# Performance work log

Measured on AMD Instinct MI355X. Metric: run time of the kernel, lower is better.

The kernel has to match this reference:

```python
import jax, jax.numpy as jnp
import numpy as np

SMOOTH = 1e-5
ALPHA = 0.25
GAMMA = 2.0
INIT_BETA = 0.5
BETA_DECAY = 0.99


def setup_inputs() -> dict:
    key = jax.random.key(0)
    ks = jax.random.split(key, 7)
    B, NC, C, H, W, D = 8, 1000, 19, 512, 512, 768
    return {
        "logits": jax.random.normal(ks[0], (B, NC), dtype=jnp.float32),
        "label": jax.random.randint(ks[1], (B,), 0, NC),
        "vision_feat": jax.random.normal(ks[2], (B, D), dtype=jnp.float32),
        "text_feat": jax.random.normal(ks[3], (B, D), dtype=jnp.float32),
        "modal_mask": jax.random.uniform(ks[4], (B, 2), dtype=jnp.float32),
        "seg_mask": jax.random.normal(ks[5], (B, C, H, W), dtype=jnp.float32),
        "seg_gt": jax.random.randint(ks[6], (B, H, W), 0, C),
        "epoch": 5,
    }


def _ce_mean(logits, label):
    logp = jax.nn.log_softmax(logits, axis=-1)
    return -jnp.take_along_axis(logp, label[:, None], axis=-1).mean()


def _dice_loss(pred, target):
    # pred: [B,C,H,W] (raw, as in the torch module), target: [B,H,W] int
    C = pred.shape[1]
    onehot = (target[:, None, :, :] == jnp.arange(C)[None, :, None, None]).astype(pred.dtype)
    inter = jnp.sum(pred * onehot, axis=(2, 3))          # [B,C]
    union = jnp.sum(pred, axis=(2, 3)) + jnp.sum(onehot, axis=(2, 3))
    dice = (2.0 * inter + SMOOTH) / (union + SMOOTH)
    return jnp.mean(1.0 - dice)


def _focal_loss(pred, target):
    # pred: [B,C,H,W] logits over class axis 1
    logp = jax.nn.log_softmax(pred, axis=1)
    logp_t = jnp.take_along_axis(logp, target[:, None, :, :], axis=1)[:, 0]  # [B,H,W]
    p_t = jnp.exp(logp_t)
    ce = -logp_t
    return jnp.mean(ALPHA * (1.0 - p_t) ** GAMMA * ce)


def _modal_balance(vision_feat, text_feat, modal_mask, epoch):
    beta_t = INIT_BETA * BETA_DECAY ** epoch
    vn = vision_feat / jnp.linalg.norm(vision_feat, axis=1, keepdims=True)
    tn = text_feat / jnp.linalg.norm(text_feat, axis=1, keepdims=True)
    v_cons = jnp.mean((vn - vn.mean(axis=0, keepdims=True)) ** 2)
    t_cons = jnp.mean((tn - tn.mean(axis=0, keepdims=True)) ** 2)
    cross = 1.0 - jnp.mean(jnp.sum(vn * tn, axis=1))  # cosine sim of unit vectors
    return ((1.0 - beta_t) * v_cons * modal_mask[:, 0].mean()
            + beta_t * t_cons * modal_mask[:, 1].mean() + cross)


def reference(logits, label, vision_feat, text_feat, modal_mask, seg_mask, seg_gt, epoch):
    ce = _ce_mean(logits, label)
    mb = _modal_balance(vision_feat, text_feat, modal_mask, epoch)
    seg = _dice_loss(seg_mask, seg_gt) + _focal_loss(seg_mask, seg_gt)
    total = ce + 0.3 * mb + 0.5 * seg
    return total
```

## Files before the change

kernel.cpp:

```cpp
#include <hip/hip_runtime.h>
#include <math.h>

#define SMOOTH_F 1e-5f
#define ALPHA_F 0.25f

constexpr int Bn = 8;
constexpr int NCn = 1000;
constexpr int Cn = 19;
constexpr int HWn = 512 * 512;
constexpr int Dn = 768;
constexpr int BC = Bn * Cn;

constexpr int TPB = 256;
constexpr int G4 = HWn / 4;
constexpr int BLKS_PER_B = G4 / TPB;
constexpr int SEG_BLOCKS = Bn * BLKS_PER_B;

constexpr int PLANE = SEG_BLOCKS;
constexpr int NPLANES = 3 * Cn + 1;
constexpr int WS_CE = NPLANES * PLANE;
constexpr int WS_MB = WS_CE + 1;

__device__ __forceinline__ float wave_sum(float v) {
#pragma unroll
  for (int off = 32; off > 0; off >>= 1) v += __shfl_down(v, off, 64);
  return v;
}
__device__ __forceinline__ float wave_max(float v) {
#pragma unroll
  for (int off = 32; off > 0; off >>= 1) v = fmaxf(v, __shfl_down(v, off, 64));
  return v;
}

__global__ __launch_bounds__(TPB, 4) void k_seg(
    const float* __restrict__ pred, const int* __restrict__ gt,
    const float* __restrict__ logits, const int* __restrict__ label,
    const float* __restrict__ vf, const float* __restrict__ tf,
    const float* __restrict__ mmask, const int* __restrict__ epoch,
    float* __restrict__ ws) {
  __shared__ float s_inter[Cn];
  __shared__ float s_count[Cn];
  __shared__ float s_pred[Cn];
  __shared__ float s_red[4];
  __shared__ float sA[4];
  __shared__ float sBv[4];
  __shared__ float nv[Bn];
  __shared__ float nt[Bn];

  const int tid = threadIdx.x;
  const int wid = tid >> 6, lane = tid & 63;
  const int blk = blockIdx.x;

  if (blk < 2) {
    if (blk == 0) {
      float acc = 0.0f;
      for (int b = 0; b < Bn; ++b) {
        const float* row = logits + b * NCn;
        float lm = -INFINITY;
        for (int j = tid; j < NCn; j += TPB) lm = fmaxf(lm, row[j]);
        lm = wave_max(lm);
        if (lane == 0) sA[wid] = lm;
        __syncthreads();
        float bm = fmaxf(fmaxf(sA[0], sA[1]), fmaxf(sA[2], sA[3]));
        __syncthreads();
        float ls = 0.0f;
        for (int j = tid; j < NCn; j += TPB) ls += expf(row[j] - bm);
        ls = wave_sum(ls);
        if (lane == 0) sA[wid] = ls;
        __syncthreads();
        if (tid == 0) {
          float lse = bm + logf(sA[0] + sA[1] + sA[2] + sA[3]);
          acc += row[label[b]] - lse;
        }
        __syncthreads();
      }
      if (tid == 0) ws[WS_CE] = -(acc / (float)Bn);
    } else {
      for (int b = 0; b < Bn; ++b) {
        float sv = 0.0f, st = 0.0f;
        for (int j = tid; j < Dn; j += TPB) {
          float a = vf[b * Dn + j];
          float c = tf[b * Dn + j];
          sv += a * a;
          st += c * c;
        }
        sv = wave_sum(sv);
        st = wave_sum(st);
        if (lane == 0) { sA[wid] = sv; sBv[wid] = st; }
        __syncthreads();
        if (tid == 0) {
          nv[b] = sqrtf(sA[0] + sA[1] + sA[2] + sA[3]);
          nt[b] = sqrtf(sBv[0] + sBv[1] + sBv[2] + sBv[3]);
        }
        __syncthreads();
      }
      float colv = 0.0f, colt = 0.0f, cross = 0.0f;
      for (int j = tid; j < Dn; j += TPB) {
        float sv = 0.0f, ssv = 0.0f, stt = 0.0f, sst = 0.0f, cr = 0.0f;
        for (int b = 0; b < Bn; ++b) {
          float vn = vf[b * Dn + j] / nv[b];
          float tn = tf[b * Dn + j] / nt[b];
          sv += vn; ssv += vn * vn;
          stt += tn; sst += tn * tn;
          cr += vn * tn;
        }
        colv += ssv - sv * sv * 0.125f;
        colt += sst - stt * stt * 0.125f;
        cross += cr;
      }
      colv = wave_sum(colv);
      colt = wave_sum(colt);
      cross = wave_sum(cross);
      if (lane == 0) { sA[wid] = colv; sBv[wid] = colt; s_red[wid] = cross; }
      __syncthreads();
      if (tid == 0) {
        float cv = sA[0] + sA[1] + sA[2] + sA[3];
        float ct = sBv[0] + sBv[1] + sBv[2] + sBv[3];
        float cr = s_red[0] + s_red[1] + s_red[2] + s_red[3];
        float v_cons = cv / (float)(Bn * Dn);
        float t_cons = ct / (float)(Bn * Dn);
        float crossv = 1.0f - cr * 0.125f;
        float beta = 0.5f * powf(0.99f, (float)epoch[0]);
        float mm0 = 0.0f, mm1 = 0.0f;
        for (int b = 0; b < Bn; ++b) { mm0 += mmask[b * 2]; mm1 += mmask[b * 2 + 1]; }
        mm0 *= 0.125f; mm1 *= 0.125f;
        ws[WS_MB] = (1.0f - beta) * v_cons * mm0 + beta * t_cons * mm1 + crossv;
      }
    }
    return;
  }

  const int sblk = blk - 2;
  const int b = sblk >> 8;
  const int grp = ((sblk & 255) << 8) + tid;

  const float* base = pred + (size_t)b * Cn * HWn;
  const int* gbase = gt + (size_t)b * HWn;
  const unsigned int goff = ((unsigned int)grp) << 4;

  if (tid < Cn) { s_inter[tid] = 0.0f; s_count[tid] = 0.0f; s_pred[tid] = 0.0f; }
  __syncthreads();

  int4 t4;
  float4 x[Cn];
  asm volatile("global_load_dwordx4 %0, %1, %2"
               : "=v"(t4) : "v"(goff), "s"(gbase));
#pragma unroll
  for (int c = 0; c < Cn; ++c) {
    const unsigned int off = goff + (unsigned int)c * (unsigned int)(HWn * 4);
    asm volatile("global_load_dwordx4 %0, %1, %2"
                 : "=v"(x[c]) : "v"(off), "s"(base));
  }
  asm volatile("s_waitcnt vmcnt(0)");
  __builtin_amdgcn_sched_barrier(0);

  float4 se = make_float4(0.0f, 0.0f, 0.0f, 0.0f);
  float4 xt = make_float4(0.0f, 0.0f, 0.0f, 0.0f);
  float psum[Cn];
#pragma unroll
  for (int c = 0; c < Cn; ++c) {
    const float4 v = x[c];
    psum[c] = v.x + v.y + v.z + v.w;
    se.x += __expf(v.x);
    se.y += __expf(v.y);
    se.z += __expf(v.z);
    se.w += __expf(v.w);
    if (t4.x == c) xt.x = v.x;
    if (t4.y == c) xt.y = v.y;
    if (t4.z == c) xt.z = v.z;
    if (t4.w == c) xt.w = v.w;
  }

  float focal = 0.0f;
#pragma unroll
  for (int j = 0; j < 4; ++j) {
    const float sej = (j == 0) ? se.x : (j == 1) ? se.y : (j == 2) ? se.z : se.w;
    const float xtj = (j == 0) ? xt.x : (j == 1) ? xt.y : (j == 2) ? xt.z : xt.w;
    const int t     = (j == 0) ? t4.x : (j == 1) ? t4.y : (j == 2) ? t4.z : t4.w;
    const float lpt = xtj - __logf(sej);
    const float p = __expf(lpt);
    const float om = 1.0f - p;
    focal += om * om * (-lpt);
    atomicAdd(&s_inter[t], xtj);
    atomicAdd(&s_count[t], 1.0f);
  }

#pragma unroll
  for (int c = 0; c < Cn; ++c) {
    float pc = wave_sum(psum[c]);
    if (lane == 0) atomicAdd(&s_pred[c], pc);
  }
  const float fw = wave_sum(focal * ALPHA_F);
  if (lane == 0) s_red[wid] = fw;
  __syncthreads();

  if (tid < Cn) {
    ws[(size_t)tid * PLANE + sblk] = s_inter[tid];
    ws[(size_t)(Cn + tid) * PLANE + sblk] = s_pred[tid];
    ws[(size_t)(2 * Cn + tid) * PLANE + sblk] = s_count[tid];
  }
  if (tid == 0)
    ws[(size_t)(3 * Cn) * PLANE + sblk] = s_red[0] + s_red[1] + s_red[2] + s_red[3];
}

__global__ __launch_bounds__(1024) void k_final(
    const float* __restrict__ ws, float* __restrict__ out) {
  __shared__ float s_part[912];
  __shared__ float s_d[3];
  __shared__ float s_f;
  const int tid = threadIdx.x;
  const int wid = tid >> 6, lane = tid & 63;

  if (tid < 2 * 3 * BC) {
    const int job = tid >> 1;
    const int half = tid & 1;
    const int quant = job / BC;
    const int pair = job - quant * BC;
    const int b = pair / Cn;
    const int c = pair - b * Cn;
    const float4* p = (const float4*)(ws + (size_t)(quant * Cn + c) * PLANE +
                                      b * 256 + half * 128);
    float s = 0.0f;
#pragma unroll 8
    for (int k = 0; k < 32; ++k) {
      const float4 v = p[k];
      s += v.x + v.y + v.z + v.w;
    }
    s_part[tid] = s;
  }
  if (wid == 15) {
    const float4* p = (const float4*)(ws + (size_t)(3 * Cn) * PLANE) + lane * 8;
    float f = 0.0f;
#pragma unroll
    for (int k = 0; k < 8; ++k) {
      const float4 v = p[k];
      f += v.x + v.y + v.z + v.w;
    }
    f = wave_sum(f);
    if (lane == 0) s_f = f;
  }
  __syncthreads();

  float v = 0.0f;
  if (tid < BC) {
    const float inter = s_part[(0 * BC + tid) * 2] + s_part[(0 * BC + tid) * 2 + 1];
    const float ps    = s_part[(1 * BC + tid) * 2] + s_part[(1 * BC + tid) * 2 + 1];
    const float cnt   = s_part[(2 * BC + tid) * 2] + s_part[(2 * BC + tid) * 2 + 1];
    const float dice = (2.0f * inter + SMOOTH_F) / (ps + cnt + SMOOTH_F);
    v = 1.0f - dice;
  }
  v = wave_sum(v);
  if (lane == 0 && wid < 3) s_d[wid] = v;
  __syncthreads();

  if (tid == 0) {
    const float dice_mean = (s_d[0] + s_d[1] + s_d[2]) / (float)BC;
    const float focal_mean = s_f / (float)(Bn * HWn);
    const float seg = dice_mean + focal_mean;
    out[0] = ws[WS_CE] + 0.3f * ws[WS_MB] + 0.5f * seg;
  }
}

extern "C" void kernel_launch(void* const* d_in, const int* in_sizes, int n_in,
                              void* d_out, int out_size, void* d_ws, size_t ws_size,
                              hipStream_t stream) {
  const float* logits = (const float*)d_in[0];
  const int* label    = (const int*)d_in[1];
  const float* vf     = (const float*)d_in[2];
  const float* tf     = (const float*)d_in[3];
  const float* mmask  = (const float*)d_in[4];
  const float* seg    = (const float*)d_in[5];
  const int* gt       = (const int*)d_in[6];
  const int* epoch    = (const int*)d_in[7];
  float* out = (float*)d_out;
  float* ws = (float*)d_ws;

  hipLaunchKernelGGL(k_seg, dim3(SEG_BLOCKS + 2), dim3(TPB), 0, stream,
                     seg, gt, logits, label, vf, tf, mmask, epoch, ws);
  hipLaunchKernelGGL(k_final, dim3(1), dim3(1024), 0, stream, ws, out);
}
```

Measured before the change: 261.1 us.

## Double-buffer seg loads across four chunks per block and move CE/MB into final kernel

Each segmentation block now processes four chunks of pixels instead of one. It uses two register buffers, so the next chunk's loads are in flight while the current chunk is computed. This cuts the grid from 2048 to 512 blocks and shrinks the per-block partial planes that the final kernel reduces. The small CE and modal-balance computations move from two special blocks of the main kernel into spare waves of the single-block final kernel. The double buffer roughly doubles register pressure (occupancy hint lowered to 2 per SIMD), and the final kernel now serially runs the CE and MB work.

After: 291.9 us. 11.8% more time.

```diff
diff --git a/kernel.cpp b/kernel.cpp
--- a/kernel.cpp
+++ b/kernel.cpp
@@ -12,14 +12,14 @@
 constexpr int BC = Bn * Cn;
 
 constexpr int TPB = 256;
+constexpr int NCHUNK = 4;
 constexpr int G4 = HWn / 4;
-constexpr int BLKS_PER_B = G4 / TPB;
+constexpr int GRPS_PER_BLK = TPB * NCHUNK;
+constexpr int BLKS_PER_B = G4 / GRPS_PER_BLK;
 constexpr int SEG_BLOCKS = Bn * BLKS_PER_B;
 
 constexpr int PLANE = SEG_BLOCKS;
 constexpr int NPLANES = 3 * Cn + 1;
-constexpr int WS_CE = NPLANES * PLANE;
-constexpr int WS_MB = WS_CE + 1;
 
 __device__ __forceinline__ float wave_sum(float v) {
 #pragma unroll
@@ -32,158 +32,96 @@
   return v;
 }
 
-__global__ __launch_bounds__(TPB, 4) void k_seg(
+__global__ __launch_bounds__(TPB, 2) void k_seg(
     const float* __restrict__ pred, const int* __restrict__ gt,
-    const float* __restrict__ logits, const int* __restrict__ label,
-    const float* __restrict__ vf, const float* __restrict__ tf,
-    const float* __restrict__ mmask, const int* __restrict__ epoch,
     float* __restrict__ ws) {
   __shared__ float s_inter[Cn];
   __shared__ float s_count[Cn];
   __shared__ float s_pred[Cn];
   __shared__ float s_red[4];
-  __shared__ float sA[4];
-  __shared__ float sBv[4];
-  __shared__ float nv[Bn];
-  __shared__ float nt[Bn];
 
   const int tid = threadIdx.x;
   const int wid = tid >> 6, lane = tid & 63;
-  const int blk = blockIdx.x;
-
-  if (blk < 2) {
-    if (blk == 0) {
-      float acc = 0.0f;
-      for (int b = 0; b < Bn; ++b) {
-        const float* row = logits + b * NCn;
-        float lm = -INFINITY;
-        for (int j = tid; j < NCn; j += TPB) lm = fmaxf(lm, row[j]);
-        lm = wave_max(lm);
-        if (lane == 0) sA[wid] = lm;
-        __syncthreads();
-        float bm = fmaxf(fmaxf(sA[0], sA[1]), fmaxf(sA[2], sA[3]));
-        __syncthreads();
-        float ls = 0.0f;
-        for (int j = tid; j < NCn; j += TPB) ls += expf(row[j] - bm);
-        ls = wave_sum(ls);
-        if (lane == 0) sA[wid] = ls;
-        __syncthreads();
-        if (tid == 0) {
-          float lse = bm + logf(sA[0] + sA[1] + sA[2] + sA[3]);
-          acc += row[label[b]] - lse;
-        }
-        __syncthreads();
-      }
-      if (tid == 0) ws[WS_CE] = -(acc / (float)Bn);
-    } else {
-      for (int b = 0; b < Bn; ++b) {
-        float sv = 0.0f, st = 0.0f;
-        for (int j = tid; j < Dn; j += TPB) {
-          float a = vf[b * Dn + j];
-          float c = tf[b * Dn + j];
-          sv += a * a;
-          st += c * c;
-        }
-        sv = wave_sum(sv);
-        st = wave_sum(st);
-        if (lane == 0) { sA[wid] = sv; sBv[wid] = st; }
-        __syncthreads();
-        if (tid == 0) {
-          nv[b] = sqrtf(sA[0] + sA[1] + sA[2] + sA[3]);
-          nt[b] = sqrtf(sBv[0] + sBv[1] + sBv[2] + sBv[3]);
-        }
-        __syncthreads();
-      }
-      float colv = 0.0f, colt = 0.0f, cross = 0.0f;
-      for (int j = tid; j < Dn; j += TPB) {
-        float sv = 0.0f, ssv = 0.0f, stt = 0.0f, sst = 0.0f, cr = 0.0f;
-        for (int b = 0; b < Bn; ++b) {
-          float vn = vf[b * Dn + j] / nv[b];
-          float tn = tf[b * Dn + j] / nt[b];
-          sv += vn; ssv += vn * vn;
-          stt += tn; sst += tn * tn;
-          cr += vn * tn;
-        }
-        colv += ssv - sv * sv * 0.125f;
-        colt += sst - stt * stt * 0.125f;
-        cross += cr;
-      }
-      colv = wave_sum(colv);
-      colt = wave_sum(colt);
-      cross = wave_sum(cross);
-      if (lane == 0) { sA[wid] = colv; sBv[wid] = colt; s_red[wid] = cross; }
-      __syncthreads();
-      if (tid == 0) {
-        float cv = sA[0] + sA[1] + sA[2] + sA[3];
-        float ct = sBv[0] + sBv[1] + sBv[2] + sBv[3];
-        float cr = s_red[0] + s_red[1] + s_red[2] + s_red[3];
-        float v_cons = cv / (float)(Bn * Dn);
-        float t_cons = ct / (float)(Bn * Dn);
-        float crossv = 1.0f - cr * 0.125f;
-        float beta = 0.5f * powf(0.99f, (float)epoch[0]);
-        float mm0 = 0.0f, mm1 = 0.0f;
-        for (int b = 0; b < Bn; ++b) { mm0 += mmask[b * 2]; mm1 += mmask[b * 2 + 1]; }
-        mm0 *= 0.125f; mm1 *= 0.125f;
-        ws[WS_MB] = (1.0f - beta) * v_cons * mm0 + beta * t_cons * mm1 + crossv;
-      }
-    }
-    return;
-  }
-
-  const int sblk = blk - 2;
-  const int b = sblk >> 8;
-  const int grp = ((sblk & 255) << 8) + tid;
-
-  const float* base = pred + (size_t)b * Cn * HWn;
-  const int* gbase = gt + (size_t)b * HWn;
-  const unsigned int goff = ((unsigned int)grp) << 4;
+  const int sblk = blockIdx.x;
+  const int b = sblk >> 6;
+  const unsigned gbase4 = (unsigned)(sblk & 63) * GRPS_PER_BLK;
+
+  const float* pbase = pred + (size_t)b * Cn * HWn;
+  const int* gtb = gt + (size_t)b * HWn;
 
   if (tid < Cn) { s_inter[tid] = 0.0f; s_count[tid] = 0.0f; s_pred[tid] = 0.0f; }
   __syncthreads();
 
-  int4 t4;
-  float4 x[Cn];
-  asm volatile("global_load_dwordx4 %0, %1, %2"
-               : "=v"(t4) : "v"(goff), "s"(gbase));
-#pragma unroll
-  for (int c = 0; c < Cn; ++c) {
-    const unsigned int off = goff + (unsigned int)c * (unsigned int)(HWn * 4);
+  float psum[Cn];
+#pragma unroll
+  for (int c = 0; c < Cn; ++c) psum[c] = 0.0f;
+  float focal = 0.0f;
+
+  float4 xA[Cn], xB[Cn];
+  int4 tA, tB;
+
+  auto issue = [&](float4 (&x)[Cn], int4& t4, int k) {
+    const unsigned goff = (gbase4 + (unsigned)k * TPB + (unsigned)tid) << 4;
     asm volatile("global_load_dwordx4 %0, %1, %2"
-                 : "=v"(x[c]) : "v"(off), "s"(base));
-  }
+                 : "=v"(t4) : "v"(goff), "s"(gtb));
+#pragma unroll
+    for (int c = 0; c < Cn; ++c) {
+      const unsigned off = goff + ((unsigned)c << 20);
+      asm volatile("global_load_dwordx4 %0, %1, %2"
+                   : "=v"(x[c]) : "v"(off), "s"(pbase));
+    }
+  };
+
+  auto compute = [&](const float4 (&x)[Cn], const int4& t4) {
+    float4 se = make_float4(0.0f, 0.0f, 0.0f, 0.0f);
+    float4 xt = make_float4(0.0f, 0.0f, 0.0f, 0.0f);
+#pragma unroll
+    for (int c = 0; c < Cn; ++c) {
+      const float4 v = x[c];
+      psum[c] += v.x + v.y + v.z + v.w;
+      se.x += __expf(v.x);
+      se.y += __expf(v.y);
+      se.z += __expf(v.z);
+      se.w += __expf(v.w);
+      if (t4.x == c) xt.x = v.x;
+      if (t4.y == c) xt.y = v.y;
+      if (t4.z == c) xt.z = v.z;
+      if (t4.w == c) xt.w = v.w;
+    }
+#pragma unroll
+    for (int j = 0; j < 4; ++j) {
+      const float sej = (j == 0) ? se.x : (j == 1) ? se.y : (j == 2) ? se.z : se.w;
+      const float xtj = (j == 0) ? xt.x : (j == 1) ? xt.y : (j == 2) ? xt.z : xt.w;
+      const int t     = (j == 0) ? t4.x : (j == 1) ? t4.y : (j == 2) ? t4.z : t4.w;
+      const float lpt = xtj - __logf(sej);
+      const float p = __expf(lpt);
+      const float om = 1.0f - p;
+      focal += om * om * (-lpt);
+      atomicAdd(&s_inter[t], xtj);
+      atomicAdd(&s_count[t], 1.0f);
+    }
+  };
+
+  issue(xA, tA, 0);
+  issue(xB, tB, 1);
+
+  asm volatile("s_waitcnt vmcnt(20)");
+  __builtin_amdgcn_sched_barrier(0);
+  compute(xA, tA);
+  issue(xA, tA, 2);
+
+  asm volatile("s_waitcnt vmcnt(20)");
+  __builtin_amdgcn_sched_barrier(0);
+  compute(xB, tB);
+  issue(xB, tB, 3);
+
+  asm volatile("s_waitcnt vmcnt(20)");
+  __builtin_amdgcn_sched_barrier(0);
+  compute(xA, tA);
+
   asm volatile("s_waitcnt vmcnt(0)");
   __builtin_amdgcn_sched_barrier(0);
-
-  float4 se = make_float4(0.0f, 0.0f, 0.0f, 0.0f);
-  float4 xt = make_float4(0.0f, 0.0f, 0.0f, 0.0f);
-  float psum[Cn];
-#pragma unroll
-  for (int c = 0; c < Cn; ++c) {
-    const float4 v = x[c];
-    psum[c] = v.x + v.y + v.z + v.w;
-    se.x += __expf(v.x);
-    se.y += __expf(v.y);
-    se.z += __expf(v.z);
-    se.w += __expf(v.w);
-    if (t4.x == c) xt.x = v.x;
-    if (t4.y == c) xt.y = v.y;
-    if (t4.z == c) xt.z = v.z;
-    if (t4.w == c) xt.w = v.w;
-  }
-
-  float focal = 0.0f;
-#pragma unroll
-  for (int j = 0; j < 4; ++j) {
-    const float sej = (j == 0) ? se.x : (j == 1) ? se.y : (j == 2) ? se.z : se.w;
-    const float xtj = (j == 0) ? xt.x : (j == 1) ? xt.y : (j == 2) ? xt.z : xt.w;
-    const int t     = (j == 0) ? t4.x : (j == 1) ? t4.y : (j == 2) ? t4.z : t4.w;
-    const float lpt = xtj - __logf(sej);
-    const float p = __expf(lpt);
-    const float om = 1.0f - p;
-    focal += om * om * (-lpt);
-    atomicAdd(&s_inter[t], xtj);
-    atomicAdd(&s_count[t], 1.0f);
-  }
+  compute(xB, tB);
 
 #pragma unroll
   for (int c = 0; c < Cn; ++c) {
@@ -204,48 +142,116 @@
 }
 
 __global__ __launch_bounds__(1024) void k_final(
-    const float* __restrict__ ws, float* __restrict__ out) {
-  __shared__ float s_part[912];
+    const float* __restrict__ ws, const float* __restrict__ logits,
+    const int* __restrict__ label, const float* __restrict__ vf,
+    const float* __restrict__ tf, const float* __restrict__ mmask,
+    const int* __restrict__ epoch, float* __restrict__ out) {
+  __shared__ float s_sum[3 * BC];
   __shared__ float s_d[3];
-  __shared__ float s_f;
+  __shared__ float s_f, s_ce, s_mb;
   const int tid = threadIdx.x;
   const int wid = tid >> 6, lane = tid & 63;
 
-  if (tid < 2 * 3 * BC) {
-    const int job = tid >> 1;
-    const int half = tid & 1;
-    const int quant = job / BC;
-    const int pair = job - quant * BC;
+  if (tid < 3 * BC) {
+    const int quant = tid / BC;
+    const int pair = tid - quant * BC;
     const int b = pair / Cn;
     const int c = pair - b * Cn;
     const float4* p = (const float4*)(ws + (size_t)(quant * Cn + c) * PLANE +
-                                      b * 256 + half * 128);
+                                      b * BLKS_PER_B);
     float s = 0.0f;
-#pragma unroll 8
-    for (int k = 0; k < 32; ++k) {
+#pragma unroll
+    for (int k = 0; k < 16; ++k) {
       const float4 v = p[k];
       s += v.x + v.y + v.z + v.w;
     }
-    s_part[tid] = s;
+    s_sum[tid] = s;
   }
   if (wid == 15) {
-    const float4* p = (const float4*)(ws + (size_t)(3 * Cn) * PLANE) + lane * 8;
-    float f = 0.0f;
-#pragma unroll
-    for (int k = 0; k < 8; ++k) {
-      const float4 v = p[k];
-      f += v.x + v.y + v.z + v.w;
-    }
+    const float4* p = (const float4*)(ws + (size_t)(3 * Cn) * PLANE) + lane * 2;
+    const float4 v0 = p[0], v1 = p[1];
+    float f = v0.x + v0.y + v0.z + v0.w + v1.x + v1.y + v1.z + v1.w;
     f = wave_sum(f);
     if (lane == 0) s_f = f;
   }
+  if (wid == 8) {
+    float acc = 0.0f;
+    for (int b = 0; b < Bn; ++b) {
+      const float* row = logits + b * NCn;
+      float rv[16];
+      float lm = -INFINITY;
+#pragma unroll
+      for (int k = 0; k < 16; ++k) {
+        const int j = lane + 64 * k;
+        rv[k] = (j < NCn) ? row[j] : -INFINITY;
+        lm = fmaxf(lm, rv[k]);
+      }
+      lm = wave_max(lm);
+      lm = __shfl(lm, 0, 64);
+      float ls = 0.0f;
+#pragma unroll
+      for (int k = 0; k < 16; ++k)
+        if (lane + 64 * k < NCn) ls += expf(rv[k] - lm);
+      ls = wave_sum(ls);
+      if (lane == 0) acc += row[label[b]] - (lm + logf(ls));
+    }
+    if (lane == 0) s_ce = -(acc / (float)Bn);
+  }
+  if (wid == 9) {
+    float nvv[Bn], ntt[Bn];
+    for (int b = 0; b < Bn; ++b) {
+      float sv = 0.0f, st = 0.0f;
+#pragma unroll
+      for (int k = 0; k < 12; ++k) {
+        const int j = lane + 64 * k;
+        const float a = vf[b * Dn + j];
+        const float c = tf[b * Dn + j];
+        sv += a * a;
+        st += c * c;
+      }
+      sv = wave_sum(sv);
+      st = wave_sum(st);
+      nvv[b] = sqrtf(__shfl(sv, 0, 64));
+      ntt[b] = sqrtf(__shfl(st, 0, 64));
+    }
+    float colv = 0.0f, colt = 0.0f, cross = 0.0f;
+#pragma unroll 2
+    for (int k = 0; k < 12; ++k) {
+      const int j = lane + 64 * k;
+      float sv = 0.0f, ssv = 0.0f, stt = 0.0f, sst = 0.0f, cr = 0.0f;
+#pragma unroll
+      for (int b = 0; b < Bn; ++b) {
+        const float vn = vf[b * Dn + j] / nvv[b];
+        const float tn = tf[b * Dn + j] / ntt[b];
+        sv += vn; ssv += vn * vn;
+        stt += tn; sst += tn * tn;
+        cr += vn * tn;
+      }
+      colv += ssv - sv * sv * 0.125f;
+      colt += sst - stt * stt * 0.125f;
+      cross += cr;
+    }
+    colv = wave_sum(colv);
+    colt = wave_sum(colt);
+    cross = wave_sum(cross);
+    if (lane == 0) {
+      const float v_cons = colv / (float)(Bn * Dn);
+      const float t_cons = colt / (float)(Bn * Dn);
+      const float crossv = 1.0f - cross * 0.125f;
+      const float beta = 0.5f * powf(0.99f, (float)epoch[0]);
+      float mm0 = 0.0f, mm1 = 0.0f;
+      for (int b = 0; b < Bn; ++b) { mm0 += mmask[b * 2]; mm1 += mmask[b * 2 + 1]; }
+      mm0 *= 0.125f; mm1 *= 0.125f;
+      s_mb = (1.0f - beta) * v_cons * mm0 + beta * t_cons * mm1 + crossv;
+    }
+  }
   __syncthreads();
 
   float v = 0.0f;
   if (tid < BC) {
-    const float inter = s_part[(0 * BC + tid) * 2] + s_part[(0 * BC + tid) * 2 + 1];
-    const float ps    = s_part[(1 * BC + tid) * 2] + s_part[(1 * BC + tid) * 2 + 1];
-    const float cnt   = s_part[(2 * BC + tid) * 2] + s_part[(2 * BC + tid) * 2 + 1];
+    const float inter = s_sum[0 * BC + tid];
+    const float ps    = s_sum[1 * BC + tid];
+    const float cnt   = s_sum[2 * BC + tid];
     const float dice = (2.0f * inter + SMOOTH_F) / (ps + cnt + SMOOTH_F);
     v = 1.0f - dice;
   }
@@ -257,7 +263,7 @@
     const float dice_mean = (s_d[0] + s_d[1] + s_d[2]) / (float)BC;
     const float focal_mean = s_f / (float)(Bn * HWn);
     const float seg = dice_mean + focal_mean;
-    out[0] = ws[WS_CE] + 0.3f * ws[WS_MB] + 0.5f * seg;
+    out[0] = s_ce + 0.3f * s_mb + 0.5f * seg;
   }
 }
 
@@ -275,7 +281,7 @@
   float* out = (float*)d_out;
   float* ws = (float*)d_ws;
 
-  hipLaunchKernelGGL(k_seg, dim3(SEG_BLOCKS + 2), dim3(TPB), 0, stream,
-                     seg, gt, logits, label, vf, tf, mmask, epoch, ws);
-  hipLaunchKernelGGL(k_final, dim3(1), dim3(1024), 0, stream, ws, out);
-}
+  hipLaunchKernelGGL(k_seg, dim3(SEG_BLOCKS), dim3(TPB), 0, stream, seg, gt, ws);
+  hipLaunchKernelGGL(k_final, dim3(1), dim3(1024), 0, stream,
+                     ws, logits, label, vf, tf, mmask, epoch, out);
+}
```
